# Kernel optimization log

Hardware: AMD Instinct MI355X
Metric: run time of the kernel (lower is better)

## Reference

```python
import jax, jax.numpy as jnp
import numpy as np

B, T, D = 2, 2048, 1024
H, DH = 16, 64
WINDOW = 256
SCALE = DH ** -0.5


def setup_inputs() -> dict:
    key = jax.random.key(0)
    ks = jax.random.split(key, 5)
    x = jax.random.normal(ks[0], (B, T, D), dtype=jnp.float32)
    # Linear params (y = x @ W + b form)
    w_qkv = jax.random.normal(ks[1], (D, 3 * D), dtype=jnp.float32) * (D ** -0.5)
    b_qkv = jnp.zeros((3 * D,), dtype=jnp.float32)
    w_out = jax.random.normal(ks[2], (D, D), dtype=jnp.float32) * (D ** -0.5)
    b_out = jnp.zeros((D,), dtype=jnp.float32)
    return {"x": x, "w_qkv": w_qkv, "b_qkv": b_qkv, "w_out": w_out, "b_out": b_out}


def reference(x, w_qkv, b_qkv, w_out, b_out):
    Bs, Ts, Ds = x.shape
    qkv = x @ w_qkv + b_qkv  # [B,T,3D]
    q, k, v = jnp.split(qkv, 3, axis=-1)
    # [B,H,T,dh]
    def heads(t):
        return t.reshape(Bs, Ts, H, DH).transpose(0, 2, 1, 3)
    q, k, v = heads(q), heads(k), heads(v)
    scores = jnp.einsum('bhqd,bhkd->bhqk', q, k) * SCALE
    i = jnp.arange(Ts)[:, None]
    j = jnp.arange(Ts)[None, :]
    # allowed: i - WINDOW <= j <= i  (causal + local window)
    allowed = (j <= i) & (j >= i - WINDOW)
    scores = jnp.where(allowed, scores, -jnp.inf)
    attn = jax.nn.softmax(scores, axis=-1)  # dropout is identity in eval
    out = jnp.einsum('bhqk,bhkd->bhqd', attn, v)
    out = out.transpose(0, 2, 1, 3).reshape(Bs, Ts, Ds)
    return out @ w_out + b_out
```

## Files before the change

### kernel.cpp

```cpp
#include <hip/hip_runtime.h>

#define BN 2
#define T_DIM 2048
#define D_DIM 1024
#define H_N 16
#define DH_N 64
#define WIN 256
#define NROWS (BN * T_DIM)
#define KDIM 1024

typedef __attribute__((ext_vector_type(8))) short bf16x8;
typedef __attribute__((ext_vector_type(4))) float f32x4;
typedef __attribute__((ext_vector_type(8))) unsigned short ushort8;
typedef __attribute__((ext_vector_type(4))) unsigned short u16x4;

static __device__ __forceinline__ unsigned short f2bf(float f) {
  unsigned int u = __float_as_uint(f);
  unsigned int r = (u + 0x7FFFu + ((u >> 16) & 1u)) >> 16;
  return (unsigned short)r;
}

static __device__ __forceinline__ void gl_lds16(const void* g, void* l) {
  __builtin_amdgcn_global_load_lds(
      (const __attribute__((address_space(1))) unsigned int*)g,
      (__attribute__((address_space(3))) unsigned int*)l, 16, 0, 0);
}

__global__ __launch_bounds__(256) void convert_bf(const float* __restrict__ src,
                                                  unsigned short* __restrict__ dst) {
  int i = (blockIdx.x * 256 + threadIdx.x) * 8;
  float4 a = *(const float4*)(src + i);
  float4 b = *(const float4*)(src + i + 4);
  ushort8 o;
  o[0] = f2bf(a.x); o[1] = f2bf(a.y); o[2] = f2bf(a.z); o[3] = f2bf(a.w);
  o[4] = f2bf(b.x); o[5] = f2bf(b.y); o[6] = f2bf(b.z); o[7] = f2bf(b.w);
  *(ushort8*)(dst + i) = o;
}

__global__ __launch_bounds__(256) void convert_t(const float* __restrict__ src,
                                                 unsigned short* __restrict__ dst,
                                                 int R, int C) {
  __shared__ float tile[64][65];
  const int t = threadIdx.x;
  const int bc = blockIdx.x * 64, br = blockIdx.y * 64;
#pragma unroll
  for (int i = 0; i < 16; ++i) {
    int idx = i * 256 + t;
    int r = idx >> 6, c = idx & 63;
    tile[r][c] = src[(size_t)(br + r) * C + bc + c];
  }
  __syncthreads();
#pragma unroll
  for (int i = 0; i < 16; ++i) {
    int idx = i * 256 + t;
    int r = idx >> 6, c = idx & 63;
    dst[(size_t)(bc + r) * R + br + c] = f2bf(tile[c][r]);
  }
}

__global__ __launch_bounds__(512) void gemm_qkv_p4(
    const unsigned short* __restrict__ A, const unsigned short* __restrict__ Bt,
    const float* __restrict__ bias, unsigned short* __restrict__ qo,
    unsigned short* __restrict__ ko, unsigned short* __restrict__ vto) {
  __shared__ unsigned short As[4][8192];
  __shared__ unsigned short Bs[4][6144];

  const int tid = threadIdx.x;
  const int w = tid >> 6, l = tid & 63;
  const int wr = w >> 2, wc = w & 3;
  const bool wlt4 = (w < 4);
  const int l15 = l & 15, kslc = l >> 4;

  const int id = blockIdx.x;
  const int wg = (id & 7) * 32 + (id >> 3);
  const int bx = wg & 15, by = wg >> 4;
  const int r0 = by * 256, c0 = bx * 192;

  const unsigned short* Ag = A + (size_t)r0 * KDIM;
  const unsigned short* Bg = Bt + (size_t)c0 * KDIM;

  f32x4 acc[8][3];
#pragma unroll
  for (int i = 0; i < 8; ++i)
#pragma unroll
    for (int j = 0; j < 3; ++j) acc[i][j] = (f32x4){0.f, 0.f, 0.f, 0.f};

  const int srow = l >> 2;
  const int srcslot = (l & 3) ^ ((l >> 3) & 3);

#define STAGE_Q(T, BUF)                                                        \
  do {                                                                         \
    const size_t kk0 = (size_t)(T) * 32;                                       \
    gl_lds16(Ag + (size_t)(w * 16 + srow) * KDIM + kk0 + srcslot * 8,          \
             (char*)&As[BUF][0] + w * 1024);                                   \
    gl_lds16(Ag + (size_t)(128 + w * 16 + srow) * KDIM + kk0 + srcslot * 8,    \
             (char*)&As[BUF][0] + (8 + w) * 1024);                             \
    gl_lds16(Bg + (size_t)(w * 16 + srow) * KDIM + kk0 + srcslot * 8,          \
             (char*)&Bs[BUF][0] + w * 1024);                                   \
    if (wlt4)                                                                  \
      gl_lds16(Bg + (size_t)(128 + w * 16 + srow) * KDIM + kk0 + srcslot * 8,  \
               (char*)&Bs[BUF][0] + (8 + w) * 1024);                           \
  } while (0)

#define QCOMPUTE(CB)                                                           \
  do {                                                                         \
    bf16x8 af[4], bfr[3];                                                      \
    _Pragma("unroll") for (int mi = 0; mi < 4; ++mi) {                         \
      int row = wr * 128 + mi * 16 + l15;                                      \
      af[mi] = *(const bf16x8*)((const char*)&As[CB][0] + row * 64 +           \
                                ((kslc ^ ((row >> 1) & 3)) << 4));             \
    }                                                                          \
    _Pragma("unroll") for (int ni = 0; ni < 3; ++ni) {                         \
      int row = wc * 48 + ni * 16 + l15;                                       \
      bfr[ni] = *(const bf16x8*)((const char*)&Bs[CB][0] + row * 64 +          \
                                 ((kslc ^ ((row >> 1) & 3)) << 4));            \
    }                                                                          \
    __builtin_amdgcn_s_setprio(1);                                             \
    _Pragma("unroll") for (int mi = 0; mi < 4; ++mi)                           \
        _Pragma("unroll") for (int ni = 0; ni < 3; ++ni) acc[mi][ni] =         \
            __builtin_amdgcn_mfma_f32_16x16x32_bf16(af[mi], bfr[ni],           \
                                                    acc[mi][ni], 0, 0, 0);     \
    __builtin_amdgcn_s_setprio(0);                                             \
    _Pragma("unroll") for (int mi = 0; mi < 4; ++mi) {                         \
      int row = wr * 128 + (mi + 4) * 16 + l15;                                \
      af[mi] = *(const bf16x8*)((const char*)&As[CB][0] + row * 64 +           \
                                ((kslc ^ ((row >> 1) & 3)) << 4));             \
    }                                                                          \
    __builtin_amdgcn_s_setprio(1);                                             \
    _Pragma("unroll") for (int mi = 0; mi < 4; ++mi)                           \
        _Pragma("unroll") for (int ni = 0; ni < 3; ++ni) acc[mi + 4][ni] =     \
            __builtin_amdgcn_mfma_f32_16x16x32_bf16(af[mi], bfr[ni],           \
                                                    acc[mi + 4][ni], 0, 0, 0); \
    __builtin_amdgcn_s_setprio(0);                                             \
  } while (0)

  STAGE_Q(0, 0);
  STAGE_Q(1, 1);

  for (int t = 0; t < 30; ++t) {
    STAGE_Q(t + 2, (t + 2) & 3);
    if (wlt4) asm volatile("s_waitcnt vmcnt(8)" ::: "memory");
    else      asm volatile("s_waitcnt vmcnt(6)" ::: "memory");
    __builtin_amdgcn_s_barrier();
    QCOMPUTE(t & 3);
  }
  if (wlt4) asm volatile("s_waitcnt vmcnt(4)" ::: "memory");
  else      asm volatile("s_waitcnt vmcnt(3)" ::: "memory");
  __builtin_amdgcn_s_barrier();
  QCOMPUTE(2);
  asm volatile("s_waitcnt vmcnt(0)" ::: "memory");
  __builtin_amdgcn_s_barrier();
  QCOMPUTE(3);
#undef STAGE_Q
#undef QCOMPUTE

#pragma unroll
  for (int ni = 0; ni < 3; ++ni) {
    const int col0 = c0 + wc * 48 + ni * 16;
    const int which = col0 >> 10;
    const int h = (col0 >> 6) & 15;
    const int dh = (col0 & 63) + l15;
    const float bv = bias[col0 + l15];
#pragma unroll
    for (int mi = 0; mi < 8; ++mi) {
      int row = r0 + wr * 128 + mi * 16 + (l >> 4) * 4;
      int b_ = row >> 11, t0 = row & 2047;
      if (which == 2) {
        u16x4 pk;
#pragma unroll
        for (int j = 0; j < 4; ++j) pk[j] = f2bf(acc[mi][ni][j] + bv);
        *(u16x4*)(vto + ((size_t)(b_ * H_N + h) * DH_N + dh) * T_DIM + t0) = pk;
      } else {
        float mul = (which == 0) ? 0.125f : 1.0f;
        unsigned short* dst = (which == 0) ? qo : ko;
#pragma unroll
        for (int j = 0; j < 4; ++j)
          dst[((size_t)(b_ * H_N + h) * T_DIM + t0 + j) * DH_N + dh] =
              f2bf((acc[mi][ni][j] + bv) * mul);
      }
    }
  }
}

__global__ __launch_bounds__(256) void gemm_out_p4(
    const unsigned short* __restrict__ A, const unsigned short* __restrict__ Bt,
    const float* __restrict__ bias, float* __restrict__ fo) {
  __shared__ unsigned short As[4][4096];
  __shared__ unsigned short Bs[4][4096];

  const int tid = threadIdx.x;
  const int w = tid >> 6, l = tid & 63;
  const int wr = w >> 1, wc = w & 1;
  const int l15 = l & 15, kslc = l >> 4;

  const int id = blockIdx.x;
  const int wg = (id & 7) * 32 + (id >> 3);
  const int bx = wg & 7, by = wg >> 3;
  const int r0 = by * 128, c0 = bx * 128;

  const unsigned short* Ag = A + (size_t)r0 * KDIM;
  const unsigned short* Bg = Bt + (size_t)c0 * KDIM;

  f32x4 acc[4][4];
#pragma unroll
  for (int i = 0; i < 4; ++i)
#pragma unroll
    for (int j = 0; j < 4; ++j) acc[i][j] = (f32x4){0.f, 0.f, 0.f, 0.f};

  const int srow = l >> 2;
  const int srcslot = (l & 3) ^ ((l >> 3) & 3);

#define STAGE_O(T, BUF)                                                        \
  do {                                                                         \
    const size_t kk0 = (size_t)(T) * 32;                                       \
    gl_lds16(Ag + (size_t)(w * 16 + srow) * KDIM + kk0 + srcslot * 8,          \
             (char*)&As[BUF][0] + w * 1024);                                   \
    gl_lds16(Ag + (size_t)(64 + w * 16 + srow) * KDIM + kk0 + srcslot * 8,     \
             (char*)&As[BUF][0] + (4 + w) * 1024);                             \
    gl_lds16(Bg + (size_t)(w * 16 + srow) * KDIM + kk0 + srcslot * 8,          \
             (char*)&Bs[BUF][0] + w * 1024);                                   \
    gl_lds16(Bg + (size_t)(64 + w * 16 + srow) * KDIM + kk0 + srcslot * 8,     \
             (char*)&Bs[BUF][0] + (4 + w) * 1024);                             \
  } while (0)

#define OCOMPUTE(CB)                                                           \
  do {                                                                         \
    bf16x8 af[4], bfr[4];                                                      \
    _Pragma("unroll") for (int mi = 0; mi < 4; ++mi) {                         \
      int row = wr * 64 + mi * 16 + l15;                                       \
      af[mi] = *(const bf16x8*)((const char*)&As[CB][0] + row * 64 +           \
                                ((kslc ^ ((row >> 1) & 3)) << 4));             \
    }                                                                          \
    _Pragma("unroll") for (int ni = 0; ni < 4; ++ni) {                         \
      int row = wc * 64 + ni * 16 + l15;                                       \
      bfr[ni] = *(const bf16x8*)((const char*)&Bs[CB][0] + row * 64 +          \
                                 ((kslc ^ ((row >> 1) & 3)) << 4));            \
    }                                                                          \
    __builtin_amdgcn_s_setprio(1);                                             \
    _Pragma("unroll") for (int mi = 0; mi < 4; ++mi)                           \
        _Pragma("unroll") for (int ni = 0; ni < 4; ++ni) acc[mi][ni] =         \
            __builtin_amdgcn_mfma_f32_16x16x32_bf16(af[mi], bfr[ni],           \
                                                    acc[mi][ni], 0, 0, 0);     \
    __builtin_amdgcn_s_setprio(0);                                             \
  } while (0)

  STAGE_O(0, 0);
  STAGE_O(1, 1);

  for (int t = 0; t < 30; ++t) {
    STAGE_O(t + 2, (t + 2) & 3);
    asm volatile("s_waitcnt vmcnt(8)" ::: "memory");
    __builtin_amdgcn_s_barrier();
    OCOMPUTE(t & 3);
  }
  asm volatile("s_waitcnt vmcnt(4)" ::: "memory");
  __builtin_amdgcn_s_barrier();
  OCOMPUTE(2);
  asm volatile("s_waitcnt vmcnt(0)" ::: "memory");
  __builtin_amdgcn_s_barrier();
  OCOMPUTE(3);
#undef STAGE_O
#undef OCOMPUTE

#pragma unroll
  for (int mi = 0; mi < 4; ++mi) {
#pragma unroll
    for (int ni = 0; ni < 4; ++ni) {
      int row = r0 + wr * 64 + mi * 16 + (l >> 4) * 4;
      int col = c0 + wc * 64 + ni * 16 + l15;
      float bv = bias[col];
#pragma unroll
      for (int j = 0; j < 4; ++j)
        fo[(size_t)(row + j) * D_DIM + col] = acc[mi][ni][j] + bv;
    }
  }
}

__global__ __launch_bounds__(256) void attn_mfma(
    const unsigned short* __restrict__ qbf,
    const unsigned short* __restrict__ kbf,
    const unsigned short* __restrict__ vtbf,
    unsigned short* __restrict__ ctx) {
  __shared__ unsigned short Ks[64 * 64];
  __shared__ unsigned short Vs[64 * 64];
  const int tid = threadIdx.x;
  const int w = tid >> 6, l = tid & 63;
  const int g = l >> 4, ln = l & 15;
  const int qt = blockIdx.x & 31;
  const int bh = blockIdx.x >> 5;
  const int q0 = qt * 64;
  const int q_abs = q0 + w * 16 + ln;

  const unsigned short* kp = kbf + (size_t)bh * T_DIM * DH_N;
  const unsigned short* vtp = vtbf + (size_t)bh * DH_N * T_DIM;

  bf16x8 qf0, qf1;
  {
    const unsigned short* qp = qbf + ((size_t)bh * T_DIM + q_abs) * DH_N;
    qf0 = *(const bf16x8*)(qp + g * 8);
    qf1 = *(const bf16x8*)(qp + 32 + g * 8);
  }

  f32x4 acc_o[4];
#pragma unroll
  for (int nd = 0; nd < 4; ++nd) acc_o[nd] = (f32x4){0.f, 0.f, 0.f, 0.f};
  float m = -1e30f, lsum = 0.f;

  const int kt_lo = (q0 >= WIN) ? (q0 - WIN) : 0;
  for (int kt = kt_lo; kt <= q0; kt += 64) {
    __syncthreads();
#pragma unroll
    for (int i = 0; i < 2; ++i) {
      int chunk = i * 256 + tid;
      int row = chunk >> 3, c16 = chunk & 7;
      int sc16 = c16 ^ (row & 7);
      int kap = 32 * ((row >> 4) & 1) + 8 * ((row & 15) >> 2) + 4 * (row >> 5) +
                (row & 3);
      gl_lds16(kp + (size_t)(kt + kap) * DH_N + sc16 * 8, (char*)Ks + chunk * 16);
      gl_lds16(vtp + (size_t)row * T_DIM + kt + sc16 * 8, (char*)Vs + chunk * 16);
    }
    __syncthreads();

    f32x4 sacc[4];
#pragma unroll
    for (int nk = 0; nk < 4; ++nk) sacc[nk] = (f32x4){0.f, 0.f, 0.f, 0.f};
#pragma unroll
    for (int ks = 0; ks < 2; ++ks) {
      bf16x8 qf = ks ? qf1 : qf0;
#pragma unroll
      for (int nk = 0; nk < 4; ++nk) {
        int rrow = nk * 16 + ln;
        int c16 = ks * 4 + g;
        bf16x8 kf = *(const bf16x8*)((const char*)Ks + rrow * 128 +
                                     ((c16 ^ (rrow & 7)) * 16));
        sacc[nk] = __builtin_amdgcn_mfma_f32_16x16x32_bf16(kf, qf, sacc[nk], 0, 0, 0);
      }
    }

    float p[4][4];
    float tm = -1e30f;
#pragma unroll
    for (int nk = 0; nk < 4; ++nk)
#pragma unroll
      for (int j = 0; j < 4; ++j) {
        int k_abs = kt + 32 * (nk & 1) + 8 * g + 4 * (nk >> 1) + j;
        float s = sacc[nk][j];
        bool ok = (k_abs <= q_abs) && (k_abs + WIN >= q_abs);
        s = ok ? s : -1e30f;
        p[nk][j] = s;
        tm = fmaxf(tm, s);
      }
    tm = fmaxf(tm, __shfl_xor(tm, 16, 64));
    tm = fmaxf(tm, __shfl_xor(tm, 32, 64));
    float mn = fmaxf(m, tm);
    float sc = __expf(m - mn);
    float ps = 0.f;
#pragma unroll
    for (int nk = 0; nk < 4; ++nk)
#pragma unroll
      for (int j = 0; j < 4; ++j) {
        p[nk][j] = __expf(p[nk][j] - mn);
        ps += p[nk][j];
      }
    ps += __shfl_xor(ps, 16, 64);
    ps += __shfl_xor(ps, 32, 64);
    lsum = lsum * sc + ps;
    m = mn;
#pragma unroll
    for (int nd = 0; nd < 4; ++nd) {
      acc_o[nd][0] *= sc; acc_o[nd][1] *= sc;
      acc_o[nd][2] *= sc; acc_o[nd][3] *= sc;
    }

    unsigned int pk[4][2];
#pragma unroll
    for (int nk = 0; nk < 4; ++nk) {
      pk[nk][0] = (unsigned)f2bf(p[nk][0]) | ((unsigned)f2bf(p[nk][1]) << 16);
      pk[nk][1] = (unsigned)f2bf(p[nk][2]) | ((unsigned)f2bf(p[nk][3]) << 16);
    }

#pragma unroll
    for (int ks = 0; ks < 2; ++ks) {
      union { unsigned int d[4]; bf16x8 v; } pf;
      pf.d[0] = pk[ks][0];     pf.d[1] = pk[ks][1];
      pf.d[2] = pk[2 + ks][0]; pf.d[3] = pk[2 + ks][1];
#pragma unroll
      for (int nd = 0; nd < 4; ++nd) {
        int drow = nd * 16 + ln;
        int c16 = ks * 4 + g;
        bf16x8 vf = *(const bf16x8*)((const char*)Vs + drow * 128 +
                                     ((c16 ^ (drow & 7)) * 16));
        acc_o[nd] = __builtin_amdgcn_mfma_f32_16x16x32_bf16(vf, pf.v, acc_o[nd],
                                                            0, 0, 0);
      }
    }
  }

  float inv = 1.f / lsum;
  const int b_ = bh >> 4, h = bh & 15;
  unsigned short* op = ctx + ((size_t)b_ * T_DIM + q_abs) * D_DIM + h * DH_N;
#pragma unroll
  for (int nd = 0; nd < 4; ++nd) {
    u16x4 o;
#pragma unroll
    for (int j = 0; j < 4; ++j) o[j] = f2bf(acc_o[nd][j] * inv);
    *(u16x4*)(op + nd * 16 + g * 4) = o;
  }
}

extern "C" void kernel_launch(void* const* d_in, const int* in_sizes, int n_in,
                              void* d_out, int out_size, void* d_ws,
                              size_t ws_size, hipStream_t stream) {
  const float* x = (const float*)d_in[0];
  const float* w_qkv = (const float*)d_in[1];
  const float* b_qkv = (const float*)d_in[2];
  const float* w_out = (const float*)d_in[3];
  const float* b_out = (const float*)d_in[4];
  float* out = (float*)d_out;

  const size_t per = (size_t)BN * H_N * T_DIM * DH_N;
  unsigned short* qbf = (unsigned short*)d_ws;
  unsigned short* kbf = qbf + per;
  unsigned short* vtbf = kbf + per;
  unsigned short* xbf = vtbf + per;
  unsigned short* wqkvt = xbf + (size_t)NROWS * D_DIM;
  unsigned short* woutt = wqkvt + (size_t)3 * D_DIM * D_DIM;
  unsigned short* ctxbf = woutt + (size_t)D_DIM * D_DIM;

  convert_bf<<<dim3(NROWS * D_DIM / (256 * 8)), dim3(256), 0, stream>>>(x, xbf);
  convert_t<<<dim3(3 * D_DIM / 64, D_DIM / 64), dim3(256), 0, stream>>>(
      w_qkv, wqkvt, D_DIM, 3 * D_DIM);
  convert_t<<<dim3(D_DIM / 64, D_DIM / 64), dim3(256), 0, stream>>>(
      w_out, woutt, D_DIM, D_DIM);

  gemm_qkv_p4<<<dim3(256), dim3(512), 0, stream>>>(xbf, wqkvt, b_qkv, qbf, kbf,
                                                   vtbf);

  attn_mfma<<<dim3(BN * H_N * (T_DIM / 64)), dim3(256), 0, stream>>>(
      qbf, kbf, vtbf, ctxbf);

  gemm_out_p4<<<dim3(256), dim3(256), 0, stream>>>(ctxbf, woutt, b_out, out);
}
```

Baseline: 90.10 us.

## Fuse conversion kernels, retile QKV GEMM to 128x128, double-buffer attention K/V

Merges the three fp32-to-bf16 conversion/transposition kernels into a single launch. Replaces the 256x192, 4-stage, 512-thread QKV GEMM with a 128x128, double-buffered, 256-thread version using a BK=64 step, giving 768 blocks instead of 256. Adds double buffering to the attention kernel so the next K/V tile loads while the current one is computed. The aim is fewer launches and better overlap, at the cost of a shallower prefetch pipeline and a full vmcnt(0) wait in the GEMM.

Result: slower. 93.51 us (+3.8%).

```diff
diff --git a/kernel.cpp b/kernel.cpp
--- a/kernel.cpp
+++ b/kernel.cpp
@@ -26,144 +26,155 @@
       (__attribute__((address_space(3))) unsigned int*)l, 16, 0, 0);
 }
 
-__global__ __launch_bounds__(256) void convert_bf(const float* __restrict__ src,
-                                                  unsigned short* __restrict__ dst) {
-  int i = (blockIdx.x * 256 + threadIdx.x) * 8;
-  float4 a = *(const float4*)(src + i);
-  float4 b = *(const float4*)(src + i + 4);
-  ushort8 o;
-  o[0] = f2bf(a.x); o[1] = f2bf(a.y); o[2] = f2bf(a.z); o[3] = f2bf(a.w);
-  o[4] = f2bf(b.x); o[5] = f2bf(b.y); o[6] = f2bf(b.z); o[7] = f2bf(b.w);
-  *(ushort8*)(dst + i) = o;
-}
-
-__global__ __launch_bounds__(256) void convert_t(const float* __restrict__ src,
-                                                 unsigned short* __restrict__ dst,
-                                                 int R, int C) {
-  __shared__ float tile[64][65];
+#define MFMA16(a, b, c) __builtin_amdgcn_mfma_f32_16x16x32_bf16(a, b, c, 0, 0, 0)
+
+static __device__ __forceinline__ void transpose_tile(
+    const float* __restrict__ src, unsigned short* __restrict__ dst, int R,
+    int C, int bx, int by, float* tile ) {
   const int t = threadIdx.x;
-  const int bc = blockIdx.x * 64, br = blockIdx.y * 64;
+  const int bc = bx * 64, br = by * 64;
 #pragma unroll
   for (int i = 0; i < 16; ++i) {
     int idx = i * 256 + t;
     int r = idx >> 6, c = idx & 63;
-    tile[r][c] = src[(size_t)(br + r) * C + bc + c];
+    tile[r * 65 + c] = src[(size_t)(br + r) * C + bc + c];
   }
   __syncthreads();
 #pragma unroll
   for (int i = 0; i < 16; ++i) {
     int idx = i * 256 + t;
     int r = idx >> 6, c = idx & 63;
-    dst[(size_t)(bc + r) * R + br + c] = f2bf(tile[c][r]);
-  }
-}
-
-__global__ __launch_bounds__(512) void gemm_qkv_p4(
+    dst[(size_t)(bc + r) * R + br + c] = f2bf(tile[c * 65 + r]);
+  }
+}
+
+__global__ __launch_bounds__(256) void convert_all(
+    const float* __restrict__ x, const float* __restrict__ w_qkv,
+    const float* __restrict__ w_out, unsigned short* __restrict__ xbf,
+    unsigned short* __restrict__ wqkvt, unsigned short* __restrict__ woutt) {
+  __shared__ float tile[64 * 65];
+  const int id = blockIdx.x;
+  if (id < 2048) {
+    int i = (id * 256 + threadIdx.x) * 8;
+    float4 a = *(const float4*)(x + i);
+    float4 b = *(const float4*)(x + i + 4);
+    ushort8 o;
+    o[0] = f2bf(a.x); o[1] = f2bf(a.y); o[2] = f2bf(a.z); o[3] = f2bf(a.w);
+    o[4] = f2bf(b.x); o[5] = f2bf(b.y); o[6] = f2bf(b.z); o[7] = f2bf(b.w);
+    *(ushort8*)(xbf + i) = o;
+  } else if (id < 2816) {
+    int j = id - 2048;
+    transpose_tile(w_qkv, wqkvt, D_DIM, 3 * D_DIM, j % 48, j / 48, tile);
+  } else {
+    int j = id - 2816;
+    transpose_tile(w_out, woutt, D_DIM, D_DIM, j % 16, j / 16, tile);
+  }
+}
+
+__global__ __launch_bounds__(256) void gemm_qkv_db(
     const unsigned short* __restrict__ A, const unsigned short* __restrict__ Bt,
     const float* __restrict__ bias, unsigned short* __restrict__ qo,
     unsigned short* __restrict__ ko, unsigned short* __restrict__ vto) {
-  __shared__ unsigned short As[4][8192];
-  __shared__ unsigned short Bs[4][6144];
+  __shared__ unsigned short As[2][128 * 64];
+  __shared__ unsigned short Bs[2][128 * 64];
 
   const int tid = threadIdx.x;
   const int w = tid >> 6, l = tid & 63;
-  const int wr = w >> 2, wc = w & 3;
-  const bool wlt4 = (w < 4);
+  const int wr = w >> 1, wc = w & 1;
   const int l15 = l & 15, kslc = l >> 4;
 
   const int id = blockIdx.x;
-  const int wg = (id & 7) * 32 + (id >> 3);
-  const int bx = wg & 15, by = wg >> 4;
-  const int r0 = by * 256, c0 = bx * 192;
+  const int wg = (id & 7) * 96 + (id >> 3);
+  const int bx = wg % 24, by = wg / 24;
+  const int r0 = by * 128, c0 = bx * 128;
 
   const unsigned short* Ag = A + (size_t)r0 * KDIM;
   const unsigned short* Bg = Bt + (size_t)c0 * KDIM;
 
-  f32x4 acc[8][3];
-#pragma unroll
-  for (int i = 0; i < 8; ++i)
-#pragma unroll
-    for (int j = 0; j < 3; ++j) acc[i][j] = (f32x4){0.f, 0.f, 0.f, 0.f};
-
-  const int srow = l >> 2;
-  const int srcslot = (l & 3) ^ ((l >> 3) & 3);
-
-#define STAGE_Q(T, BUF)                                                        \
+  f32x4 acc[4][4];
+#pragma unroll
+  for (int i = 0; i < 4; ++i)
+#pragma unroll
+    for (int j = 0; j < 4; ++j) acc[i][j] = (f32x4){0.f, 0.f, 0.f, 0.f};
+
+  const int grow = tid >> 3;
+  const int gcol = (tid & 7) ^ (grow & 7);
+
+#define STG(T, BUF)                                                            \
   do {                                                                         \
-    const size_t kk0 = (size_t)(T) * 32;                                       \
-    gl_lds16(Ag + (size_t)(w * 16 + srow) * KDIM + kk0 + srcslot * 8,          \
-             (char*)&As[BUF][0] + w * 1024);                                   \
-    gl_lds16(Ag + (size_t)(128 + w * 16 + srow) * KDIM + kk0 + srcslot * 8,    \
-             (char*)&As[BUF][0] + (8 + w) * 1024);                             \
-    gl_lds16(Bg + (size_t)(w * 16 + srow) * KDIM + kk0 + srcslot * 8,          \
-             (char*)&Bs[BUF][0] + w * 1024);                                   \
-    if (wlt4)                                                                  \
-      gl_lds16(Bg + (size_t)(128 + w * 16 + srow) * KDIM + kk0 + srcslot * 8,  \
-               (char*)&Bs[BUF][0] + (8 + w) * 1024);                           \
+    const size_t kk0 = (size_t)(T) * 64;                                       \
+    _Pragma("unroll") for (int ch = 0; ch < 4; ++ch) {                         \
+      gl_lds16(Ag + (size_t)(ch * 32 + grow) * KDIM + kk0 + gcol * 8,          \
+               (char*)&As[BUF][0] + ch * 4096 + w * 1024);                     \
+      gl_lds16(Bg + (size_t)(ch * 32 + grow) * KDIM + kk0 + gcol * 8,          \
+               (char*)&Bs[BUF][0] + ch * 4096 + w * 1024);                     \
+    }                                                                          \
   } while (0)
 
-#define QCOMPUTE(CB)                                                           \
+#define LDA(CB, mi, ks)                                                        \
+  (*(const bf16x8*)((const char*)&As[CB][0] +                                  \
+                    (wr * 64 + (mi)*16 + l15) * 128 +                          \
+                    ((((ks)*4 + kslc) ^ (l15 & 7)) << 4)))
+#define LDB(CB, ni, ks)                                                        \
+  (*(const bf16x8*)((const char*)&Bs[CB][0] +                                  \
+                    (wc * 64 + (ni)*16 + l15) * 128 +                          \
+                    ((((ks)*4 + kslc) ^ (l15 & 7)) << 4)))
+
+#define HALF(CB, ks)                                                           \
   do {                                                                         \
-    bf16x8 af[4], bfr[3];                                                      \
-    _Pragma("unroll") for (int mi = 0; mi < 4; ++mi) {                         \
-      int row = wr * 128 + mi * 16 + l15;                                      \
-      af[mi] = *(const bf16x8*)((const char*)&As[CB][0] + row * 64 +           \
-                                ((kslc ^ ((row >> 1) & 3)) << 4));             \
-    }                                                                          \
-    _Pragma("unroll") for (int ni = 0; ni < 3; ++ni) {                         \
-      int row = wc * 48 + ni * 16 + l15;                                       \
-      bfr[ni] = *(const bf16x8*)((const char*)&Bs[CB][0] + row * 64 +          \
-                                 ((kslc ^ ((row >> 1) & 3)) << 4));            \
-    }                                                                          \
+    bf16x8 a0 = LDA(CB, 0, ks), a1 = LDA(CB, 1, ks), a2 = LDA(CB, 2, ks),      \
+           a3 = LDA(CB, 3, ks);                                                \
+    bf16x8 b0 = LDB(CB, 0, ks), b1 = LDB(CB, 1, ks), b2 = LDB(CB, 2, ks),      \
+           b3 = LDB(CB, 3, ks);                                                \
     __builtin_amdgcn_s_setprio(1);                                             \
-    _Pragma("unroll") for (int mi = 0; mi < 4; ++mi)                           \
-        _Pragma("unroll") for (int ni = 0; ni < 3; ++ni) acc[mi][ni] =         \
-            __builtin_amdgcn_mfma_f32_16x16x32_bf16(af[mi], bfr[ni],           \
-                                                    acc[mi][ni], 0, 0, 0);     \
-    __builtin_amdgcn_s_setprio(0);                                             \
-    _Pragma("unroll") for (int mi = 0; mi < 4; ++mi) {                         \
-      int row = wr * 128 + (mi + 4) * 16 + l15;                                \
-      af[mi] = *(const bf16x8*)((const char*)&As[CB][0] + row * 64 +           \
-                                ((kslc ^ ((row >> 1) & 3)) << 4));             \
-    }                                                                          \
-    __builtin_amdgcn_s_setprio(1);                                             \
-    _Pragma("unroll") for (int mi = 0; mi < 4; ++mi)                           \
-        _Pragma("unroll") for (int ni = 0; ni < 3; ++ni) acc[mi + 4][ni] =     \
-            __builtin_amdgcn_mfma_f32_16x16x32_bf16(af[mi], bfr[ni],           \
-                                                    acc[mi + 4][ni], 0, 0, 0); \
+    acc[0][0] = MFMA16(a0, b0, acc[0][0]);                                     \
+    acc[0][1] = MFMA16(a0, b1, acc[0][1]);                                     \
+    acc[0][2] = MFMA16(a0, b2, acc[0][2]);                                     \
+    acc[0][3] = MFMA16(a0, b3, acc[0][3]);                                     \
+    acc[1][0] = MFMA16(a1, b0, acc[1][0]);                                     \
+    acc[1][1] = MFMA16(a1, b1, acc[1][1]);                                     \
+    acc[1][2] = MFMA16(a1, b2, acc[1][2]);                                     \
+    acc[1][3] = MFMA16(a1, b3, acc[1][3]);                                     \
+    acc[2][0] = MFMA16(a2, b0, acc[2][0]);                                     \
+    acc[2][1] = MFMA16(a2, b1, acc[2][1]);                                     \
+    acc[2][2] = MFMA16(a2, b2, acc[2][2]);                                     \
+    acc[2][3] = MFMA16(a2, b3, acc[2][3]);                                     \
+    acc[3][0] = MFMA16(a3, b0, acc[3][0]);                                     \
+    acc[3][1] = MFMA16(a3, b1, acc[3][1]);                                     \
+    acc[3][2] = MFMA16(a3, b2, acc[3][2]);                                     \
+    acc[3][3] = MFMA16(a3, b3, acc[3][3]);                                     \
     __builtin_amdgcn_s_setprio(0);                                             \
   } while (0)
 
-  STAGE_Q(0, 0);
-  STAGE_Q(1, 1);
-
-  for (int t = 0; t < 30; ++t) {
-    STAGE_Q(t + 2, (t + 2) & 3);
-    if (wlt4) asm volatile("s_waitcnt vmcnt(8)" ::: "memory");
-    else      asm volatile("s_waitcnt vmcnt(6)" ::: "memory");
+  STG(0, 0);
+#pragma unroll 2
+  for (int t = 0; t < 15; ++t) {
+    const int cb = t & 1;
+    asm volatile("s_waitcnt vmcnt(0)" ::: "memory");
     __builtin_amdgcn_s_barrier();
-    QCOMPUTE(t & 3);
-  }
-  if (wlt4) asm volatile("s_waitcnt vmcnt(4)" ::: "memory");
-  else      asm volatile("s_waitcnt vmcnt(3)" ::: "memory");
-  __builtin_amdgcn_s_barrier();
-  QCOMPUTE(2);
+    STG(t + 1, cb ^ 1);
+    HALF(cb, 0);
+    HALF(cb, 1);
+  }
   asm volatile("s_waitcnt vmcnt(0)" ::: "memory");
   __builtin_amdgcn_s_barrier();
-  QCOMPUTE(3);
-#undef STAGE_Q
-#undef QCOMPUTE
-
-#pragma unroll
-  for (int ni = 0; ni < 3; ++ni) {
-    const int col0 = c0 + wc * 48 + ni * 16;
+  HALF(1, 0);
+  HALF(1, 1);
+#undef STG
+#undef LDA
+#undef LDB
+#undef HALF
+
+#pragma unroll
+  for (int ni = 0; ni < 4; ++ni) {
+    const int col0 = c0 + wc * 64 + ni * 16;
     const int which = col0 >> 10;
     const int h = (col0 >> 6) & 15;
     const int dh = (col0 & 63) + l15;
     const float bv = bias[col0 + l15];
 #pragma unroll
-    for (int mi = 0; mi < 8; ++mi) {
-      int row = r0 + wr * 128 + mi * 16 + (l >> 4) * 4;
+    for (int mi = 0; mi < 4; ++mi) {
+      int row = r0 + wr * 64 + mi * 16 + (l >> 4) * 4;
       int b_ = row >> 11, t0 = row & 2047;
       if (which == 2) {
         u16x4 pk;
@@ -239,8 +250,7 @@
     __builtin_amdgcn_s_setprio(1);                                             \
     _Pragma("unroll") for (int mi = 0; mi < 4; ++mi)                           \
         _Pragma("unroll") for (int ni = 0; ni < 4; ++ni) acc[mi][ni] =         \
-            __builtin_amdgcn_mfma_f32_16x16x32_bf16(af[mi], bfr[ni],           \
-                                                    acc[mi][ni], 0, 0, 0);     \
+            MFMA16(af[mi], bfr[ni], acc[mi][ni]);                              \
     __builtin_amdgcn_s_setprio(0);                                             \
   } while (0)
 
@@ -281,8 +291,8 @@
     const unsigned short* __restrict__ kbf,
     const unsigned short* __restrict__ vtbf,
     unsigned short* __restrict__ ctx) {
-  __shared__ unsigned short Ks[64 * 64];
-  __shared__ unsigned short Vs[64 * 64];
+  __shared__ unsigned short Ks[2][64 * 64];
+  __shared__ unsigned short Vs[2][64 * 64];
   const int tid = threadIdx.x;
   const int w = tid >> 6, l = tid & 63;
   const int g = l >> 4, ln = l & 15;
@@ -301,25 +311,40 @@
     qf1 = *(const bf16x8*)(qp + 32 + g * 8);
   }
 
+  const int srow = tid >> 2, sc16a = (tid & 3) ^ (srow & 7);
+  const int srow2 = srow + 64 >> 0;
+#define KAP(row) \
+  (32 * (((row) >> 4) & 1) + 8 * (((row)&15) >> 2) + 4 * ((row) >> 5) + ((row)&3))
+
+#define STAGEKV(KT, BUF)                                                       \
+  do {                                                                         \
+    _Pragma("unroll") for (int i_ = 0; i_ < 2; ++i_) {                         \
+      int chunk = i_ * 256 + tid;                                              \
+      int row = chunk >> 3, c16 = chunk & 7;                                   \
+      int sc16 = c16 ^ (row & 7);                                              \
+      int kap = KAP(row);                                                      \
+      gl_lds16(kp + (size_t)((KT) + kap) * DH_N + sc16 * 8,                    \
+               (char*)&Ks[BUF][0] + chunk * 16);                               \
+      gl_lds16(vtp + (size_t)row * T_DIM + (KT) + sc16 * 8,                    \
+               (char*)&Vs[BUF][0] + chunk * 16);                               \
+    }                                                                          \
+  } while (0)
+
   f32x4 acc_o[4];
 #pragma unroll
   for (int nd = 0; nd < 4; ++nd) acc_o[nd] = (f32x4){0.f, 0.f, 0.f, 0.f};
   float m = -1e30f, lsum = 0.f;
 
   const int kt_lo = (q0 >= WIN) ? (q0 - WIN) : 0;
-  for (int kt = kt_lo; kt <= q0; kt += 64) {
-    __syncthreads();
-#pragma unroll
-    for (int i = 0; i < 2; ++i) {
-      int chunk = i * 256 + tid;
-      int row = chunk >> 3, c16 = chunk & 7;
-      int sc16 = c16 ^ (row & 7);
-      int kap = 32 * ((row >> 4) & 1) + 8 * ((row & 15) >> 2) + 4 * (row >> 5) +
-                (row & 3);
-      gl_lds16(kp + (size_t)(kt + kap) * DH_N + sc16 * 8, (char*)Ks + chunk * 16);
-      gl_lds16(vtp + (size_t)row * T_DIM + kt + sc16 * 8, (char*)Vs + chunk * 16);
-    }
-    __syncthreads();
+  const int nt = ((q0 - kt_lo) >> 6) + 1;
+
+  STAGEKV(kt_lo, 0);
+  for (int i = 0; i < nt; ++i) {
+    const int cb = i & 1;
+    const int kt = kt_lo + i * 64;
+    asm volatile("s_waitcnt vmcnt(0)" ::: "memory");
+    __builtin_amdgcn_s_barrier();
+    if (i + 1 < nt) STAGEKV(kt + 64, cb ^ 1);
 
     f32x4 sacc[4];
 #pragma unroll
@@ -331,9 +356,9 @@
       for (int nk = 0; nk < 4; ++nk) {
         int rrow = nk * 16 + ln;
         int c16 = ks * 4 + g;
-        bf16x8 kf = *(const bf16x8*)((const char*)Ks + rrow * 128 +
+        bf16x8 kf = *(const bf16x8*)((const char*)&Ks[cb][0] + rrow * 128 +
                                      ((c16 ^ (rrow & 7)) * 16));
-        sacc[nk] = __builtin_amdgcn_mfma_f32_16x16x32_bf16(kf, qf, sacc[nk], 0, 0, 0);
+        sacc[nk] = MFMA16(kf, qf, sacc[nk]);
       }
     }
 
@@ -388,13 +413,14 @@
       for (int nd = 0; nd < 4; ++nd) {
         int drow = nd * 16 + ln;
         int c16 = ks * 4 + g;
-        bf16x8 vf = *(const bf16x8*)((const char*)Vs + drow * 128 +
+        bf16x8 vf = *(const bf16x8*)((const char*)&Vs[cb][0] + drow * 128 +
                                      ((c16 ^ (drow & 7)) * 16));
-        acc_o[nd] = __builtin_amdgcn_mfma_f32_16x16x32_bf16(vf, pf.v, acc_o[nd],
-                                                            0, 0, 0);
+        acc_o[nd] = MFMA16(vf, pf.v, acc_o[nd]);
       }
     }
   }
+#undef STAGEKV
+#undef KAP
 
   float inv = 1.f / lsum;
   const int b_ = bh >> 4, h = bh & 15;
@@ -427,13 +453,10 @@
   unsigned short* woutt = wqkvt + (size_t)3 * D_DIM * D_DIM;
   unsigned short* ctxbf = woutt + (size_t)D_DIM * D_DIM;
 
-  convert_bf<<<dim3(NROWS * D_DIM / (256 * 8)), dim3(256), 0, stream>>>(x, xbf);
-  convert_t<<<dim3(3 * D_DIM / 64, D_DIM / 64), dim3(256), 0, stream>>>(
-      w_qkv, wqkvt, D_DIM, 3 * D_DIM);
-  convert_t<<<dim3(D_DIM / 64, D_DIM / 64), dim3(256), 0, stream>>>(
-      w_out, woutt, D_DIM, D_DIM);
-
-  gemm_qkv_p4<<<dim3(256), dim3(512), 0, stream>>>(xbf, wqkvt, b_qkv, qbf, kbf,
+  convert_all<<<dim3(3072), dim3(256), 0, stream>>>(x, w_qkv, w_out, xbf,
+                                                    wqkvt, woutt);
+
+  gemm_qkv_db<<<dim3(768), dim3(256), 0, stream>>>(xbf, wqkvt, b_qkv, qbf, kbf,
                                                    vtbf);
 
   attn_mfma<<<dim3(BN * H_N * (T_DIM / 64)), dim3(256), 0, stream>>>(
```
